# Performance work log

Measured on AMD Instinct MI355X. Metric: run time of the kernel, lower is better.

Reference implementation:

```python
import jax, jax.numpy as jnp
import numpy as np

E = 1024
B, QL, KVL = 8, 2048, 2048


def setup_inputs() -> dict:
    key = jax.random.key(0)
    ks = jax.random.split(key, 12)
    s = 1.0 / np.sqrt(E)
    return {
        "query": jax.random.normal(ks[0], (B, QL, E), jnp.float32),
        "key_value": jax.random.normal(ks[1], (B, KVL, E), jnp.float32),
        "attention_mask": jax.random.randint(ks[2], (B, QL, KVL), 0, 2, jnp.int32),
        "Wq": jax.random.uniform(ks[3], (E, E), jnp.float32, -s, s),
        "bq": jax.random.uniform(ks[4], (E,), jnp.float32, -s, s),
        "Wk": jax.random.uniform(ks[5], (E, E), jnp.float32, -s, s),
        "bk": jax.random.uniform(ks[6], (E,), jnp.float32, -s, s),
        "Wv": jax.random.uniform(ks[7], (E, E), jnp.float32, -s, s),
        "bv": jax.random.uniform(ks[8], (E,), jnp.float32, -s, s),
        "Wo": jax.random.uniform(ks[9], (E, E), jnp.float32, -s, s),
        "bo": jax.random.uniform(ks[10], (E,), jnp.float32, -s, s),
    }


def reference(query, key_value, attention_mask, Wq, bq, Wk, bk, Wv, bv, Wo, bo):
    # torch Linear: x @ W.T + b
    q = jnp.einsum('bqe,fe->bqf', query, Wq) + bq          # [B, QL, E]
    k = jnp.einsum('bke,fe->bkf', key_value, Wk) + bk      # [B, KVL, E]
    v = jnp.einsum('bke,fe->bkf', key_value, Wv) + bv      # [B, KVL, E]
    scale = 1.0 / jnp.sqrt(jnp.asarray(q.shape[-1], q.dtype))
    attn = jnp.einsum('bqe,bke->bqk', q, k) * scale        # [B, QL, KVL]
    attn = jnp.where(attention_mask == 0, -jnp.inf, attn)
    attn = jax.nn.softmax(attn, axis=-1)
    out = jnp.einsum('bqk,bke->bqe', attn, v)              # [B, QL, E]
    out = jnp.einsum('bqe,fe->bqf', out, Wo) + bo
    return out
```

## Files before the change

### kernel.cpp

```cpp
#include <hip/hip_runtime.h>
#include <hip/hip_bf16.h>
#include <stdint.h>

typedef unsigned short u16;
typedef short s16x8 __attribute__((ext_vector_type(8)));
typedef u16 u16x8 __attribute__((ext_vector_type(8)));
typedef u16 u16x4 __attribute__((ext_vector_type(4)));
typedef float f32x4 __attribute__((ext_vector_type(4)));

__device__ __forceinline__ u16 f2bf(float f) {
  union { float f; uint32_t u; } c; c.f = f;
  uint32_t u = c.u;
  u = u + 0x7fffu + ((u >> 16) & 1u);
  return (u16)(u >> 16);
}
__device__ __forceinline__ float bf2f(u16 b) {
  union { uint32_t u; float f; } c; c.u = ((uint32_t)b) << 16;
  return c.f;
}

__device__ __forceinline__ void gld_lds16(const u16* g, u16* l) {
  __builtin_amdgcn_global_load_lds(
      (const __attribute__((address_space(1))) uint32_t*)g,
      (__attribute__((address_space(3))) uint32_t*)l,
      16, 0, 0);
}

__global__ __launch_bounds__(256) void cvt_f32_to_bf16(
    const float* __restrict__ in, u16* __restrict__ out, long n8) {
  long i = (long)blockIdx.x * blockDim.x + threadIdx.x;
  if (i >= n8) return;
  const float4 a = ((const float4*)in)[i * 2];
  const float4 b = ((const float4*)in)[i * 2 + 1];
  u16x8 r;
  r[0] = f2bf(a.x); r[1] = f2bf(a.y); r[2] = f2bf(a.z); r[3] = f2bf(a.w);
  r[4] = f2bf(b.x); r[5] = f2bf(b.y); r[6] = f2bf(b.z); r[7] = f2bf(b.w);
  *(u16x8*)&out[i * 8] = r;
}

__global__ __launch_bounds__(256) void cvt_w4(
    const float* __restrict__ w0, const float* __restrict__ w1,
    const float* __restrict__ w2, const float* __restrict__ w3,
    u16* __restrict__ out) {
  const float* src = (blockIdx.y == 0) ? w0 : (blockIdx.y == 1) ? w1
                   : (blockIdx.y == 2) ? w2 : w3;
  const long i = (long)blockIdx.x * blockDim.x + threadIdx.x;
  const float4 a = ((const float4*)src)[i * 2];
  const float4 b = ((const float4*)src)[i * 2 + 1];
  u16x8 r;
  r[0] = f2bf(a.x); r[1] = f2bf(a.y); r[2] = f2bf(a.z); r[3] = f2bf(a.w);
  r[4] = f2bf(b.x); r[5] = f2bf(b.y); r[6] = f2bf(b.z); r[7] = f2bf(b.w);
  *(u16x8*)&out[(long)blockIdx.y * 1048576 + i * 8] = r;
}

__global__ __launch_bounds__(256) void transpose64(
    const u16* __restrict__ in, u16* __restrict__ out, int R, int C) {
  __shared__ u16 t[64][66];
  const long ib = (long)blockIdx.z * (long)R * C;
  const int r0 = blockIdx.x * 64, c0 = blockIdx.y * 64;
  const int tid = threadIdx.x;
#pragma unroll
  for (int i = 0; i < 2; ++i) {
    const int ch = i * 256 + tid;
    const int r = ch >> 3, cc = ch & 7;
    const s16x8 v = *(const s16x8*)&in[ib + (long)(r0 + r) * C + c0 + cc * 8];
#pragma unroll
    for (int j = 0; j < 8; ++j) t[r][cc * 8 + j] = (u16)v[j];
  }
  __syncthreads();
#pragma unroll
  for (int i = 0; i < 2; ++i) {
    const int ch = i * 256 + tid;
    const int c = ch >> 3, rr = ch & 7;
    u16x8 r8;
#pragma unroll
    for (int j = 0; j < 8; ++j) r8[j] = t[rr * 8 + j][c];
    *(u16x8*)&out[ib + (long)(c0 + c) * R + r0 + rr * 8] = r8;
  }
}

__global__ __launch_bounds__(256) void prep_vec(
    const float* __restrict__ Wk, const float* __restrict__ bq,
    const float* __restrict__ Wo, const float* __restrict__ bv,
    const float* __restrict__ bo, float* __restrict__ wvec,
    float* __restrict__ bvo, float scale) {
  const int bi = blockIdx.x;
  if (bi < 4) {
    const int g = bi * 256 + threadIdx.x;
    float s = 0.f;
    for (int e = 0; e < 1024; ++e) s += Wk[(long)e * 1024 + g] * bq[e];
    wvec[g] = s * scale;
  } else {
    const int f = (bi - 4) * 256 + threadIdx.x;
    const float4* row = (const float4*)&Wo[(long)f * 1024];
    float s = 0.f;
    for (int e4 = 0; e4 < 256; ++e4) {
      const float4 x = row[e4];
      const float4 b4 = ((const float4*)bv)[e4];
      s += x.x * b4.x + x.y * b4.y + x.z * b4.z + x.w * b4.w;
    }
    bvo[f] = s + bo[f];
  }
}

__global__ __launch_bounds__(256) void cgemv(
    const u16* __restrict__ kvbf, const float* __restrict__ wvec,
    float* __restrict__ c) {
  __shared__ float w[1024];
  const int tid = threadIdx.x;
#pragma unroll
  for (int i = 0; i < 4; ++i) w[i * 256 + tid] = wvec[i * 256 + tid];
  __syncthreads();
  const int lane = tid & 63, wv_ = tid >> 6;
  const long rowbase = (long)blockIdx.x * 16 + wv_ * 4;
#pragma unroll
  for (int r = 0; r < 4; ++r) {
    const long row = rowbase + r;
    const u16* p = &kvbf[row * 1024 + lane * 16];
    const u16x8 a = *(const u16x8*)p;
    const u16x8 b = *(const u16x8*)(p + 8);
    float s = 0.f;
#pragma unroll
    for (int j = 0; j < 8; ++j) s += bf2f(a[j]) * w[lane * 16 + j];
#pragma unroll
    for (int j = 0; j < 8; ++j) s += bf2f(b[j]) * w[lane * 16 + 8 + j];
#pragma unroll
    for (int off = 32; off >= 1; off >>= 1) s += __shfl_xor(s, off);
    if (lane == 0) c[row] = s;
  }
}

__global__ __launch_bounds__(256) void softmax_rows(u16* __restrict__ S) {
  const long base = (long)blockIdx.x * 2048;
  const int tid = threadIdx.x;
  const int lane = tid & 63, wave = tid >> 6;
  u16x8 raw = *(const u16x8*)&S[base + tid * 8];
  float v[8];
#pragma unroll
  for (int j = 0; j < 8; ++j) v[j] = bf2f(raw[j]);
  float m = v[0];
#pragma unroll
  for (int j = 1; j < 8; ++j) m = fmaxf(m, v[j]);
#pragma unroll
  for (int off = 32; off >= 1; off >>= 1) m = fmaxf(m, __shfl_xor(m, off));
  __shared__ float red[8];
  if (lane == 0) red[wave] = m;
  __syncthreads();
  m = fmaxf(fmaxf(red[0], red[1]), fmaxf(red[2], red[3]));
  float s = 0.f;
#pragma unroll
  for (int j = 0; j < 8; ++j) { v[j] = __expf(v[j] - m); s += v[j]; }
#pragma unroll
  for (int off = 32; off >= 1; off >>= 1) s += __shfl_xor(s, off);
  if (lane == 0) red[4 + wave] = s;
  __syncthreads();
  s = (red[4] + red[5]) + (red[6] + red[7]);
  const float inv = 1.f / s;
#pragma unroll
  for (int j = 0; j < 8; ++j) raw[j] = f2bf(v[j] * inv);
  *(u16x8*)&S[base + tid * 8] = raw;
}

union __align__(16) SmemT {
  u16 stage[2][128 * 64];
  float epi[32 * 132];
};

__device__ __forceinline__ s16x8 ldsfrag(const u16* p, int r, int c8) {
  return *(const s16x8*)&p[r * 64 + ((c8 ^ (r & 7)) << 3)];
}

__device__ __forceinline__ void stage128(const u16* __restrict__ gb, int row0,
                                         int K, int k0, u16* lbuf, int tid) {
#pragma unroll
  for (int i = 0; i < 4; ++i) {
    const int f = i * 256 + tid;
    const int rl = f >> 3, s = f & 7;
    const int gc = (s ^ (rl & 7)) << 3;
    gld_lds16(gb + (long)(row0 + rl) * K + k0 + gc, lbuf + f * 8);
  }
}

template<bool HAS_BIAS, int MODE, bool HAS_MASK>
__global__ __launch_bounds__(256, 4) void gemm128(
    const u16* __restrict__ A, const u16* __restrict__ B,
    const float* __restrict__ bias, const int* __restrict__ mask,
    void* __restrict__ Cv,
    int M, int N, int K, long sA, long sB, long sC, long sMask, long sBias,
    float scale) {
  __shared__ SmemT sm;
  const int nx = gridDim.x, ny = gridDim.y;
  const int did = blockIdx.x + nx * (blockIdx.y + ny * blockIdx.z);
  const int cpx = (nx * ny * gridDim.z) >> 3;
  const int nf = (did & 7) * cpx + (did >> 3);
  const int b = nf / (nx * ny);
  const int rr = nf % (nx * ny);
  const int bm = (rr / ny) * 128;
  const int bn = (rr % ny) * 128;

  const u16* Ab = A + (long)b * sA;
  const u16* Bb = B + (long)b * sB;
  const float* biasB = HAS_BIAS ? (bias + (long)b * sBias) : nullptr;
  const int tid = threadIdx.x;
  const int lane = tid & 63, wave = tid >> 6;
  const int wm = wave >> 1, wn = wave & 1;
  const int lr = lane & 15, lk = lane >> 4;
  const int NT = K >> 6;

  f32x4 acc[4][4] = {};

  for (int t = 0; t < NT; ++t) {
    stage128(Ab, bm, K, t << 6, sm.stage[0], tid);
    stage128(Bb, bn, K, t << 6, sm.stage[1], tid);
    asm volatile("s_waitcnt vmcnt(0)" ::: "memory");
    __syncthreads();
#pragma unroll
    for (int ks = 0; ks < 2; ++ks) {
      s16x8 af[4], bg[4];
#pragma unroll
      for (int mi = 0; mi < 4; ++mi)
        af[mi] = ldsfrag(sm.stage[0], wm * 64 + mi * 16 + lr, ks * 4 + lk);
#pragma unroll
      for (int ni = 0; ni < 4; ++ni)
        bg[ni] = ldsfrag(sm.stage[1], wn * 64 + ni * 16 + lr, ks * 4 + lk);
#pragma unroll
      for (int mi = 0; mi < 4; ++mi)
#pragma unroll
        for (int ni = 0; ni < 4; ++ni)
          acc[mi][ni] = __builtin_amdgcn_mfma_f32_16x16x32_bf16(
              af[mi], bg[ni], acc[mi][ni], 0, 0, 0);
    }
    __syncthreads();
  }

  const long cb = (long)b * sC;
  if (MODE == 3) {
#pragma unroll
    for (int mi = 0; mi < 4; ++mi) {
#pragma unroll
      for (int ni = 0; ni < 4; ++ni) {
        const int row0 = bm + wm * 64 + mi * 16 + (lk << 2);
        const int col2 = bn + wn * 64 + ni * 16 + lr;
        const float bvx = HAS_BIAS ? biasB[col2] : 0.f;
        u16x4 pk;
#pragma unroll
        for (int j = 0; j < 4; ++j) pk[j] = f2bf(acc[mi][ni][j] * scale + bvx);
        const long ad = (long)(row0 >> 11) * ((long)N * 2048) +
                        (long)col2 * 2048 + (row0 & 2047);
        *(u16x4*)&((u16*)Cv)[ad] = pk;
      }
    }
  } else {
    const int q = tid & 7, r = tid >> 3;
#pragma unroll
    for (int h = 0; h < 4; ++h) {
      __syncthreads();
      if (wm == (h >> 1)) {
        const int mi0 = (h & 1) * 2;
#pragma unroll
        for (int mm = 0; mm < 2; ++mm) {
          const int mi = mi0 + mm;
#pragma unroll
          for (int ni = 0; ni < 4; ++ni) {
            const int c = wn * 64 + ni * 16 + lr;
            const float bvx = HAS_BIAS ? biasB[bn + c] : 0.f;
#pragma unroll
            for (int j = 0; j < 4; ++j)
              sm.epi[(mm * 16 + (lk << 2) + j) * 132 + c] =
                  acc[mi][ni][j] * scale + bvx;
          }
        }
      }
      __syncthreads();
      const int growi = bm + h * 32 + r;
      const long grow = cb + (long)growi * N + bn;
      const long mrow = HAS_MASK
          ? ((long)b * sMask + (long)growi * (long)N + bn) : 0;
#pragma unroll
      for (int ch = 0; ch < 2; ++ch) {
        const int c0 = ch * 64 + q * 8;
        const float4 x = *(const float4*)&sm.epi[r * 132 + c0];
        const float4 y = *(const float4*)&sm.epi[r * 132 + c0 + 4];
        if (MODE == 1) {
          *(float4*)&((float*)Cv)[grow + c0] = x;
          *(float4*)&((float*)Cv)[grow + c0 + 4] = y;
        } else {
          u16x8 pk;
          if (HAS_MASK) {
            const int4 ma = *(const int4*)&mask[mrow + c0];
            const int4 mb = *(const int4*)&mask[mrow + c0 + 4];
            pk[0] = f2bf(ma.x ? x.x : -1e30f);
            pk[1] = f2bf(ma.y ? x.y : -1e30f);
            pk[2] = f2bf(ma.z ? x.z : -1e30f);
            pk[3] = f2bf(ma.w ? x.w : -1e30f);
            pk[4] = f2bf(mb.x ? y.x : -1e30f);
            pk[5] = f2bf(mb.y ? y.y : -1e30f);
            pk[6] = f2bf(mb.z ? y.z : -1e30f);
            pk[7] = f2bf(mb.w ? y.w : -1e30f);
          } else {
            pk[0] = f2bf(x.x); pk[1] = f2bf(x.y);
            pk[2] = f2bf(x.z); pk[3] = f2bf(x.w);
            pk[4] = f2bf(y.x); pk[5] = f2bf(y.y);
            pk[6] = f2bf(y.z); pk[7] = f2bf(y.w);
          }
          *(u16x8*)&((u16*)Cv)[grow + c0] = pk;
        }
      }
    }
  }
}

extern "C" void kernel_launch(void* const* d_in, const int* in_sizes, int n_in,
                              void* d_out, int out_size, void* d_ws, size_t ws_size,
                              hipStream_t stream) {
  const float* query = (const float*)d_in[0];
  const float* kv    = (const float*)d_in[1];
  const int*   mask  = (const int*)d_in[2];
  const float* Wq = (const float*)d_in[3];
  const float* bq = (const float*)d_in[4];
  const float* Wk = (const float*)d_in[5];
  const float* bk = (const float*)d_in[6];
  const float* Wv = (const float*)d_in[7];
  const float* bv = (const float*)d_in[8];
  const float* Wo = (const float*)d_in[9];
  const float* bo = (const float*)d_in[10];
  float* out = (float*)d_out;
  (void)bk;

  char* ws = (char*)d_ws;
  const size_t MB = (size_t)1 << 20;
  u16* qbf  = (u16*)(ws + 0);
  u16* kvbf = (u16*)(ws + 32 * MB);
  u16* wq   = (u16*)(ws + 64 * MB);
  u16* wo   = (u16*)(ws + 70 * MB);
  u16* WqT  = (u16*)(ws + 72 * MB);
  u16* WkT  = (u16*)(ws + 74 * MB);
  u16* WvT  = (u16*)(ws + 76 * MB);
  u16* Mt   = (u16*)(ws + 78 * MB);
  u16* Wvo  = (u16*)(ws + 80 * MB);
  float* wvec = (float*)(ws + 82 * MB);
  float* bvo  = (float*)(ws + 82 * MB + 65536);
  float* cvec = (float*)(ws + 83 * MB);
  u16* qM   = (u16*)(ws + 84 * MB);
  u16* VwT  = (u16*)(ws + 116 * MB);
  u16* S    = (u16*)(ws + 148 * MB);

  const long sQK = (long)2048 * 1024;
  const long sS  = (long)2048 * 2048;

  cvt_f32_to_bf16<<<8192, 256, 0, stream>>>(query, qbf, 2097152);
  cvt_f32_to_bf16<<<8192, 256, 0, stream>>>(kv, kvbf, 2097152);
  cvt_w4<<<dim3(512, 4, 1), 256, 0, stream>>>(Wq, Wk, Wv, Wo, wq);
  transpose64<<<dim3(16, 16, 3), 256, 0, stream>>>(wq, WqT, 1024, 1024);
  prep_vec<<<8, 256, 0, stream>>>(Wk, bq, Wo, bv, bo, wvec, bvo, 0.03125f);

  gemm128<false, 0, false><<<dim3(8, 8, 1), 256, 0, stream>>>(
      WkT, WqT, nullptr, nullptr, Mt, 1024, 1024, 1024, 0, 0, 0, 0, 0, 1.f);
  gemm128<false, 0, false><<<dim3(8, 8, 1), 256, 0, stream>>>(
      wo, WvT, nullptr, nullptr, Wvo, 1024, 1024, 1024, 0, 0, 0, 0, 0, 1.f);

  cgemv<<<1024, 256, 0, stream>>>(kvbf, wvec, cvec);

  gemm128<false, 0, false><<<dim3(128, 8, 1), 256, 0, stream>>>(
      qbf, Mt, nullptr, nullptr, qM, 16384, 1024, 1024, 0, 0, 0, 0, 0, 1.f);

  gemm128<false, 3, false><<<dim3(128, 8, 1), 256, 0, stream>>>(
      kvbf, Wvo, nullptr, nullptr, VwT, 16384, 1024, 1024, 0, 0, 0, 0, 0, 1.f);

  gemm128<true, 0, true><<<dim3(16, 16, 8), 256, 0, stream>>>(
      qM, kvbf, cvec, mask, S, 2048, 2048, 1024, sQK, sQK, sS, sS, 2048,
      0.03125f);

  softmax_rows<<<16384, 256, 0, stream>>>(S);

  gemm128<true, 1, false><<<dim3(16, 8, 8), 256, 0, stream>>>(
      S, VwT, bvo, nullptr, out, 2048, 1024, 2048, sS, sQK, sQK, 0, 0, 1.f);
}
```

Before: 393.7 us.

## Batch weight-fold GEMMs, replace scalar prep_vec with bf16 GEMV, drop transposed-store epilogue

Replaces the scalar fp32 prep_vec kernel with a wave-reduced bf16 GEMV over the transposed/converted weights. The two small 1024x1024 weight-fold GEMMs are merged into one batched launch using negative/positive batch strides. The V projection is recomputed as Wvo x kv^T per batch so the standard row-major epilogue produces the transposed layout directly, which lets the strided MODE 3 scatter-store epilogue be removed. This cuts launches and uncoalesced writes, at the cost of the bias vectors now coming from bf16-rounded weights.

```diff
diff --git a/kernel.cpp b/kernel.cpp
--- a/kernel.cpp
+++ b/kernel.cpp
@@ -79,27 +79,38 @@
   }
 }
 
-__global__ __launch_bounds__(256) void prep_vec(
-    const float* __restrict__ Wk, const float* __restrict__ bq,
-    const float* __restrict__ Wo, const float* __restrict__ bv,
-    const float* __restrict__ bo, float* __restrict__ wvec,
-    float* __restrict__ bvo, float scale) {
-  const int bi = blockIdx.x;
-  if (bi < 4) {
-    const int g = bi * 256 + threadIdx.x;
+__global__ __launch_bounds__(256) void bgemv(
+    const u16* __restrict__ matA, const float* __restrict__ vecA,
+    const u16* __restrict__ matB, const float* __restrict__ vecB,
+    const float* __restrict__ addB, float* __restrict__ outA,
+    float* __restrict__ outB, float scaleA) {
+  __shared__ float w[1024];
+  const int tid = threadIdx.x;
+  const bool second = blockIdx.x >= 64;
+  const u16* mat = second ? matB : matA;
+  const float* vec = second ? vecB : vecA;
+  const int rb = (second ? (int)blockIdx.x - 64 : (int)blockIdx.x) * 16;
+#pragma unroll
+  for (int i = 0; i < 4; ++i) w[i * 256 + tid] = vec[i * 256 + tid];
+  __syncthreads();
+  const int lane = tid & 63, wv_ = tid >> 6;
+#pragma unroll
+  for (int r = 0; r < 4; ++r) {
+    const int row = rb + wv_ * 4 + r;
+    const u16* p = &mat[(long)row * 1024 + lane * 16];
+    const u16x8 a = *(const u16x8*)p;
+    const u16x8 b = *(const u16x8*)(p + 8);
     float s = 0.f;
-    for (int e = 0; e < 1024; ++e) s += Wk[(long)e * 1024 + g] * bq[e];
-    wvec[g] = s * scale;
-  } else {
-    const int f = (bi - 4) * 256 + threadIdx.x;
-    const float4* row = (const float4*)&Wo[(long)f * 1024];
-    float s = 0.f;
-    for (int e4 = 0; e4 < 256; ++e4) {
-      const float4 x = row[e4];
-      const float4 b4 = ((const float4*)bv)[e4];
-      s += x.x * b4.x + x.y * b4.y + x.z * b4.z + x.w * b4.w;
+#pragma unroll
+    for (int j = 0; j < 8; ++j) s += bf2f(a[j]) * w[lane * 16 + j];
+#pragma unroll
+    for (int j = 0; j < 8; ++j) s += bf2f(b[j]) * w[lane * 16 + 8 + j];
+#pragma unroll
+    for (int off = 32; off >= 1; off >>= 1) s += __shfl_xor(s, off);
+    if (lane == 0) {
+      if (second) outB[row] = s + addB[row];
+      else        outA[row] = s * scaleA;
     }
-    bvo[f] = s + bo[f];
   }
 }
 
@@ -234,77 +245,59 @@
   }
 
   const long cb = (long)b * sC;
-  if (MODE == 3) {
-#pragma unroll
-    for (int mi = 0; mi < 4; ++mi) {
-#pragma unroll
-      for (int ni = 0; ni < 4; ++ni) {
-        const int row0 = bm + wm * 64 + mi * 16 + (lk << 2);
-        const int col2 = bn + wn * 64 + ni * 16 + lr;
-        const float bvx = HAS_BIAS ? biasB[col2] : 0.f;
-        u16x4 pk;
-#pragma unroll
-        for (int j = 0; j < 4; ++j) pk[j] = f2bf(acc[mi][ni][j] * scale + bvx);
-        const long ad = (long)(row0 >> 11) * ((long)N * 2048) +
-                        (long)col2 * 2048 + (row0 & 2047);
-        *(u16x4*)&((u16*)Cv)[ad] = pk;
+  const int q = tid & 7, r = tid >> 3;
+#pragma unroll
+  for (int h = 0; h < 4; ++h) {
+    __syncthreads();
+    if (wm == (h >> 1)) {
+      const int mi0 = (h & 1) * 2;
+#pragma unroll
+      for (int mm = 0; mm < 2; ++mm) {
+        const int mi = mi0 + mm;
+#pragma unroll
+        for (int ni = 0; ni < 4; ++ni) {
+          const int c = wn * 64 + ni * 16 + lr;
+          const float bvx = HAS_BIAS ? biasB[bn + c] : 0.f;
+#pragma unroll
+          for (int j = 0; j < 4; ++j)
+            sm.epi[(mm * 16 + (lk << 2) + j) * 132 + c] =
+                acc[mi][ni][j] * scale + bvx;
+        }
       }
     }
-  } else {
-    const int q = tid & 7, r = tid >> 3;
-#pragma unroll
-    for (int h = 0; h < 4; ++h) {
-      __syncthreads();
-      if (wm == (h >> 1)) {
-        const int mi0 = (h & 1) * 2;
-#pragma unroll
-        for (int mm = 0; mm < 2; ++mm) {
-          const int mi = mi0 + mm;
-#pragma unroll
-          for (int ni = 0; ni < 4; ++ni) {
-            const int c = wn * 64 + ni * 16 + lr;
-            const float bvx = HAS_BIAS ? biasB[bn + c] : 0.f;
-#pragma unroll
-            for (int j = 0; j < 4; ++j)
-              sm.epi[(mm * 16 + (lk << 2) + j) * 132 + c] =
-                  acc[mi][ni][j] * scale + bvx;
-          }
+    __syncthreads();
+    const int growi = bm + h * 32 + r;
+    const long grow = cb + (long)growi * N + bn;
+    const long mrow = HAS_MASK
+        ? ((long)b * sMask + (long)growi * (long)N + bn) : 0;
+#pragma unroll
+    for (int ch = 0; ch < 2; ++ch) {
+      const int c0 = ch * 64 + q * 8;
+      const float4 x = *(const float4*)&sm.epi[r * 132 + c0];
+      const float4 y = *(const float4*)&sm.epi[r * 132 + c0 + 4];
+      if (MODE == 1) {
+        *(float4*)&((float*)Cv)[grow + c0] = x;
+        *(float4*)&((float*)Cv)[grow + c0 + 4] = y;
+      } else {
+        u16x8 pk;
+        if (HAS_MASK) {
+          const int4 ma = *(const int4*)&mask[mrow + c0];
+          const int4 mb = *(const int4*)&mask[mrow + c0 + 4];
+          pk[0] = f2bf(ma.x ? x.x : -1e30f);
+          pk[1] = f2bf(ma.y ? x.y : -1e30f);
+          pk[2] = f2bf(ma.z ? x.z : -1e30f);
+          pk[3] = f2bf(ma.w ? x.w : -1e30f);
+          pk[4] = f2bf(mb.x ? y.x : -1e30f);
+          pk[5] = f2bf(mb.y ? y.y : -1e30f);
+          pk[6] = f2bf(mb.z ? y.z : -1e30f);
+          pk[7] = f2bf(mb.w ? y.w : -1e30f);
+        } else {
+          pk[0] = f2bf(x.x); pk[1] = f2bf(x.y);
+          pk[2] = f2bf(x.z); pk[3] = f2bf(x.w);
+          pk[4] = f2bf(y.x); pk[5] = f2bf(y.y);
+          pk[6] = f2bf(y.z); pk[7] = f2bf(y.w);
         }
-      }
-      __syncthreads();
-      const int growi = bm + h * 32 + r;
-      const long grow = cb + (long)growi * N + bn;
-      const long mrow = HAS_MASK
-          ? ((long)b * sMask + (long)growi * (long)N + bn) : 0;
-#pragma unroll
-      for (int ch = 0; ch < 2; ++ch) {
-        const int c0 = ch * 64 + q * 8;
-        const float4 x = *(const float4*)&sm.epi[r * 132 + c0];
-        const float4 y = *(const float4*)&sm.epi[r * 132 + c0 + 4];
-        if (MODE == 1) {
-          *(float4*)&((float*)Cv)[grow + c0] = x;
-          *(float4*)&((float*)Cv)[grow + c0 + 4] = y;
-        } else {
-          u16x8 pk;
-          if (HAS_MASK) {
-            const int4 ma = *(const int4*)&mask[mrow + c0];
-            const int4 mb = *(const int4*)&mask[mrow + c0 + 4];
-            pk[0] = f2bf(ma.x ? x.x : -1e30f);
-            pk[1] = f2bf(ma.y ? x.y : -1e30f);
-            pk[2] = f2bf(ma.z ? x.z : -1e30f);
-            pk[3] = f2bf(ma.w ? x.w : -1e30f);
-            pk[4] = f2bf(mb.x ? y.x : -1e30f);
-            pk[5] = f2bf(mb.y ? y.y : -1e30f);
-            pk[6] = f2bf(mb.z ? y.z : -1e30f);
-            pk[7] = f2bf(mb.w ? y.w : -1e30f);
-          } else {
-            pk[0] = f2bf(x.x); pk[1] = f2bf(x.y);
-            pk[2] = f2bf(x.z); pk[3] = f2bf(x.w);
-            pk[4] = f2bf(y.x); pk[5] = f2bf(y.y);
-            pk[6] = f2bf(y.z); pk[7] = f2bf(y.w);
-          }
-          *(u16x8*)&((u16*)Cv)[grow + c0] = pk;
-        }
+        *(u16x8*)&((u16*)Cv)[grow + c0] = pk;
       }
     }
   }
@@ -335,7 +328,6 @@
   u16* wo   = (u16*)(ws + 70 * MB);
   u16* WqT  = (u16*)(ws + 72 * MB);
   u16* WkT  = (u16*)(ws + 74 * MB);
-  u16* WvT  = (u16*)(ws + 76 * MB);
   u16* Mt   = (u16*)(ws + 78 * MB);
   u16* Wvo  = (u16*)(ws + 80 * MB);
   float* wvec = (float*)(ws + 82 * MB);
@@ -352,20 +344,19 @@
   cvt_f32_to_bf16<<<8192, 256, 0, stream>>>(kv, kvbf, 2097152);
   cvt_w4<<<dim3(512, 4, 1), 256, 0, stream>>>(Wq, Wk, Wv, Wo, wq);
   transpose64<<<dim3(16, 16, 3), 256, 0, stream>>>(wq, WqT, 1024, 1024);
-  prep_vec<<<8, 256, 0, stream>>>(Wk, bq, Wo, bv, bo, wvec, bvo, 0.03125f);
-
-  gemm128<false, 0, false><<<dim3(8, 8, 1), 256, 0, stream>>>(
-      WkT, WqT, nullptr, nullptr, Mt, 1024, 1024, 1024, 0, 0, 0, 0, 0, 1.f);
-  gemm128<false, 0, false><<<dim3(8, 8, 1), 256, 0, stream>>>(
-      wo, WvT, nullptr, nullptr, Wvo, 1024, 1024, 1024, 0, 0, 0, 0, 0, 1.f);
-
+  bgemv<<<128, 256, 0, stream>>>(WkT, bq, wo, bv, bo, wvec, bvo, 0.03125f);
   cgemv<<<1024, 256, 0, stream>>>(kvbf, wvec, cvec);
+
+  gemm128<false, 0, false><<<dim3(8, 8, 2), 256, 0, stream>>>(
+      WkT, WqT, nullptr, nullptr, Mt, 1024, 1024, 1024,
+      -2097152L, 2097152L, 1048576L, 0, 0, 1.f);
 
   gemm128<false, 0, false><<<dim3(128, 8, 1), 256, 0, stream>>>(
       qbf, Mt, nullptr, nullptr, qM, 16384, 1024, 1024, 0, 0, 0, 0, 0, 1.f);
 
-  gemm128<false, 3, false><<<dim3(128, 8, 1), 256, 0, stream>>>(
-      kvbf, Wvo, nullptr, nullptr, VwT, 16384, 1024, 1024, 0, 0, 0, 0, 0, 1.f);
+  gemm128<false, 0, false><<<dim3(8, 16, 8), 256, 0, stream>>>(
+      Wvo, kvbf, nullptr, nullptr, VwT, 1024, 2048, 1024,
+      0, sQK, sQK, 0, 0, 1.f);
 
   gemm128<true, 0, true><<<dim3(16, 16, 8), 256, 0, stream>>>(
       qM, kvbf, cvec, mask, S, 2048, 2048, 1024, sQK, sQK, sS, sS, 2048,
```

Result: faster. 338.1 us (-14.1%).
